# Performance work log

Measured on AMD Instinct MI355X. Metric: run time of the kernel, lower is better.

## Reference

```python
import jax, jax.numpy as jnp
import numpy as np

EMBED_DIM = 1024
NUM_HEADS = 16
HEAD_DIM = EMBED_DIM // NUM_HEADS
B, T = 4, 2048


def setup_inputs() -> dict:
    key = jax.random.key(0)
    ks = jax.random.split(key, 5)
    s = 1.0 / np.sqrt(EMBED_DIM)
    x = jax.random.normal(ks[0], (B, T, EMBED_DIM), dtype=jnp.float32)
    W_qkv = jax.random.uniform(ks[1], (EMBED_DIM, 3 * EMBED_DIM), minval=-s, maxval=s, dtype=jnp.float32)
    b_qkv = jax.random.uniform(ks[2], (3 * EMBED_DIM,), minval=-s, maxval=s, dtype=jnp.float32)
    W_proj = jax.random.uniform(ks[3], (EMBED_DIM, EMBED_DIM), minval=-s, maxval=s, dtype=jnp.float32)
    b_proj = jax.random.uniform(ks[4], (EMBED_DIM,), minval=-s, maxval=s, dtype=jnp.float32)
    return {"x": x, "W_qkv": W_qkv, "b_qkv": b_qkv, "W_proj": W_proj, "b_proj": b_proj}


def reference(x, W_qkv, b_qkv, W_proj, b_proj):
    Bq, Tq, C = x.shape
    H, D = NUM_HEADS, HEAD_DIM
    qkv = x @ W_qkv + b_qkv                      # [B,T,3C]
    qkv = qkv.reshape(Bq, Tq, 3, H, D)
    q = qkv[:, :, 0].transpose(0, 2, 1, 3)       # [B,H,T,D]
    k = qkv[:, :, 1].transpose(0, 2, 1, 3)
    v = qkv[:, :, 2].transpose(0, 2, 1, 3)
    scale = 1.0 / jnp.sqrt(jnp.asarray(D, x.dtype))
    attn = jnp.einsum('bhqd,bhkd->bhqk', q, k) * scale  # [B,H,T,T]
    mask = jnp.tril(jnp.ones((Tq, Tq), dtype=bool))     # causal: keep lower triangle
    attn = jnp.where(mask, attn, jnp.asarray(-jnp.inf, attn.dtype))
    attn = jax.nn.softmax(attn, axis=-1)
    out = jnp.einsum('bhqk,bhkd->bhqd', attn, v)        # [B,H,T,D]
    out = out.transpose(0, 2, 1, 3).reshape(Bq, Tq, C)
    return out @ W_proj + b_proj
```

## Files before the change

### kernel.cpp

```cpp
#include <hip/hip_runtime.h>
#include <stdint.h>

typedef unsigned short ushort_t;
typedef __attribute__((ext_vector_type(4))) unsigned int  u32x4;
typedef __attribute__((ext_vector_type(2))) unsigned int  u32x2;
typedef __attribute__((ext_vector_type(4))) float         f32x4;
typedef __attribute__((ext_vector_type(8))) __bf16        bf16x8;
typedef __attribute__((ext_vector_type(2))) __bf16        bf16x2;

__device__ __forceinline__ ushort_t f2bf(float f) {
    unsigned int u = __float_as_uint(f);
    u += 0x7fffu + ((u >> 16) & 1u);
    return (ushort_t)(u >> 16);
}
__device__ __forceinline__ unsigned int pack2bf(float a, float b) {
    return (unsigned int)f2bf(a) | ((unsigned int)f2bf(b) << 16);
}
#if __has_builtin(__builtin_amdgcn_cvt_pk_bf16_f32)
__device__ __forceinline__ unsigned int pack2bf_fast(float a, float b) {
    bf16x2 v = __builtin_amdgcn_cvt_pk_bf16_f32(a, b);
    return __builtin_bit_cast(unsigned int, v);
}
#else
__device__ __forceinline__ unsigned int pack2bf_fast(float a, float b) {
    return pack2bf(a, b);
}
#endif
__device__ __forceinline__ f32x4 mfma16(bf16x8 a, bf16x8 b, f32x4 c) {
    return __builtin_amdgcn_mfma_f32_16x16x32_bf16(a, b, c, 0, 0, 0);
}
__device__ __forceinline__ bf16x8 ldfrag(const ushort_t* p) {
    return __builtin_bit_cast(bf16x8, *(const u32x4*)p);
}

__device__ __forceinline__ void wg_barrier() {
    asm volatile("s_waitcnt lgkmcnt(0)\n\ts_barrier" ::: "memory");
}

#define QSCALE 0.18033688011112042f

__global__ __launch_bounds__(256) void xcast(const float* __restrict__ X,
                                             ushort_t* __restrict__ Xb) {
    long i = ((long)blockIdx.x * 256 + threadIdx.x) * 8;
    float4 a = *(const float4*)(X + i);
    float4 b = *(const float4*)(X + i + 4);
    u32x4 pk;
    pk.x = pack2bf(a.x, a.y); pk.y = pack2bf(a.z, a.w);
    pk.z = pack2bf(b.x, b.y); pk.w = pack2bf(b.z, b.w);
    *(u32x4*)(Xb + i) = pk;
}

__global__ __launch_bounds__(256) void wt_kernel(const float* __restrict__ W,
                                                 ushort_t* __restrict__ Wt,
                                                 int K, int N) {
    __shared__ float tile[32][33];
    int tx = threadIdx.x, ty = threadIdx.y;
    int n0 = blockIdx.x * 32, k0 = blockIdx.y * 32;
    for (int p = 0; p < 4; ++p)
        tile[ty + 8*p][tx] = W[(long)(k0 + ty + 8*p) * N + n0 + tx];
    __syncthreads();
    for (int p = 0; p < 4; ++p)
        Wt[(long)(n0 + ty + 8*p) * K + k0 + tx] = f2bf(tile[tx][ty + 8*p]);
}

__global__ __launch_bounds__(256) void gemm_qkv(const ushort_t* __restrict__ Xb,
                                                const ushort_t* __restrict__ Wt,
                                                const float* __restrict__ bias,
                                                ushort_t* __restrict__ Qo,
                                                ushort_t* __restrict__ Ko,
                                                ushort_t* __restrict__ Vto) {
    __shared__ __align__(16) ushort_t smem[128 * 136];

    const int tid  = threadIdx.x;
    const int g    = blockIdx.x;
    const int grp  = g / 192, rr = g % 192;
    const int m0   = (grp * 8 + (rr & 7)) * 128;
    const int n0   = (rr >> 3) * 128;
    const int lane = tid & 63, w = tid >> 6;
    const int quad = lane >> 4, l16 = lane & 15;
    const int wm = (w >> 1) * 64, wn = (w & 1) * 64;

    const int srow  = tid >> 2;
    const int slot  = tid & 3;
    const int oct   = slot ^ ((tid >> 3) & 3);
    const int wofs  = srow * 32 + slot * 8;
    const int rslot = (quad ^ ((l16 >> 1) & 3)) * 8;

    const ushort_t* Ap = Xb + (long)(m0 + srow) * 1024 + oct * 8;
    const ushort_t* Bp = Wt + (long)(n0 + srow) * 1024 + oct * 8;

    f32x4 acc[4][4] = {};

    u32x4 AA0 = *(const u32x4*)(Ap);
    u32x4 AA1 = *(const u32x4*)(Ap + 65536);
    u32x4 BA0 = *(const u32x4*)(Bp);
    u32x4 BA1 = *(const u32x4*)(Bp + 65536);
    u32x4 AB0 = *(const u32x4*)(Ap + 32);
    u32x4 AB1 = *(const u32x4*)(Ap + 32 + 65536);
    u32x4 BB0 = *(const u32x4*)(Bp + 32);
    u32x4 BB1 = *(const u32x4*)(Bp + 32 + 65536);

    for (int k0 = 0; k0 < 1024; k0 += 64) {
        {
            ushort_t* As = smem;
            ushort_t* Bs = smem + 8192;
            *(u32x4*)&As[wofs]        = AA0;
            *(u32x4*)&As[wofs + 2048] = AA1;
            *(u32x4*)&Bs[wofs]        = BA0;
            *(u32x4*)&Bs[wofs + 2048] = BA1;
            int kf = (k0 + 64 < 1024) ? k0 + 64 : k0;
            AA0 = *(const u32x4*)(Ap + kf);
            AA1 = *(const u32x4*)(Ap + kf + 65536);
            BA0 = *(const u32x4*)(Bp + kf);
            BA1 = *(const u32x4*)(Bp + kf + 65536);
            wg_barrier();
            bf16x8 af[4], bfr[4];
            for (int i = 0; i < 4; ++i)
                af[i] = ldfrag(&As[(wm + 16*i + l16) * 32 + rslot]);
            for (int j = 0; j < 4; ++j)
                bfr[j] = ldfrag(&Bs[(wn + 16*j + l16) * 32 + rslot]);
            for (int i = 0; i < 4; ++i)
                for (int j = 0; j < 4; ++j)
                    acc[i][j] = mfma16(af[i], bfr[j], acc[i][j]);
        }
        {
            ushort_t* As = smem + 4096;
            ushort_t* Bs = smem + 8192 + 4096;
            *(u32x4*)&As[wofs]        = AB0;
            *(u32x4*)&As[wofs + 2048] = AB1;
            *(u32x4*)&Bs[wofs]        = BB0;
            *(u32x4*)&Bs[wofs + 2048] = BB1;
            int kf = (k0 + 96 < 1024) ? k0 + 96 : k0 + 32;
            AB0 = *(const u32x4*)(Ap + kf);
            AB1 = *(const u32x4*)(Ap + kf + 65536);
            BB0 = *(const u32x4*)(Bp + kf);
            BB1 = *(const u32x4*)(Bp + kf + 65536);
            wg_barrier();
            bf16x8 af[4], bfr[4];
            for (int i = 0; i < 4; ++i)
                af[i] = ldfrag(&As[(wm + 16*i + l16) * 32 + rslot]);
            for (int j = 0; j < 4; ++j)
                bfr[j] = ldfrag(&Bs[(wn + 16*j + l16) * 32 + rslot]);
            for (int i = 0; i < 4; ++i)
                for (int j = 0; j < 4; ++j)
                    acc[i][j] = mfma16(af[i], bfr[j], acc[i][j]);
        }
    }

    float bj[4];
    for (int j = 0; j < 4; ++j) bj[j] = bias[n0 + wn + 16*j + l16];
    const int bb = m0 >> 11, t0m = m0 & 2047;
    __syncthreads();

    if (n0 < 2048) {
        ushort_t* dst = (n0 < 1024) ? Qo : Ko;
        const float scale = (n0 < 1024) ? QSCALE : 1.0f;
        const int nbase = (n0 < 1024) ? n0 : n0 - 1024;
        for (int i = 0; i < 4; ++i)
            for (int j = 0; j < 4; ++j) {
                int nl = wn + 16*j + l16;
                for (int r = 0; r < 4; ++r) {
                    int ml = wm + 16*i + quad*4 + r;
                    smem[ml * 136 + nl] = f2bf((acc[i][j][r] + bj[j]) * scale);
                }
            }
        __syncthreads();
        for (int c = 0; c < 8; ++c) {
            int chunk = tid + 256 * c;
            int row = chunk >> 4, nc = (chunk & 15) * 8;
            int n = nbase + nc;
            int hh = n >> 6, d = n & 63;
            *(u32x4*)&dst[((long)(bb*16 + hh) * 2048 + t0m + row) * 64 + d] =
                *(const u32x4*)&smem[row * 136 + nc];
        }
    } else {
        for (int i = 0; i < 4; ++i)
            for (int j = 0; j < 4; ++j) {
                int nl = wn + 16*j + l16;
                for (int r = 0; r < 4; ++r) {
                    int ml = wm + 16*i + quad*4 + r;
                    smem[nl * 136 + ml] = f2bf(acc[i][j][r] + bj[j]);
                }
            }
        __syncthreads();
        for (int c = 0; c < 8; ++c) {
            int chunk = tid + 256 * c;
            int row = chunk >> 4, mc = (chunk & 15) * 8;
            int n = n0 - 2048 + row;
            int hh = n >> 6, d = n & 63;
            *(u32x4*)&Vto[((long)(bb*16 + hh) * 64 + d) * 2048 + t0m + mc] =
                *(const u32x4*)&smem[row * 136 + mc];
        }
    }
}

__global__ __launch_bounds__(256) void attn_kernel(const ushort_t* __restrict__ Q,
                                                   const ushort_t* __restrict__ K,
                                                   const ushort_t* __restrict__ Vt,
                                                   ushort_t* __restrict__ O) {
    __shared__ __align__(16) ushort_t Ks[2][64 * 64];
    __shared__ __align__(16) ushort_t Vs[2][64 * 64];
    __shared__ __align__(16) ushort_t Ps[128 * 72];

    const int tid  = threadIdx.x;
    const int lane = tid & 63, w = tid >> 6, quad = lane >> 4, l16 = lane & 15;
    const int g    = blockIdx.x;
    const int bh   = (g & 7) + 8 * ((g >> 3) & 7);
    const int qt   = 15 - (g >> 6);
    const ushort_t* qptr = Q  + (long)bh * 2048 * 64;
    const ushort_t* kptr = K  + (long)bh * 2048 * 64;
    const ushort_t* vptr = Vt + (long)bh * 64 * 2048;
    const int bb2 = bh >> 4, h = bh & 15;

    const int srow = tid >> 3;
    const int slot = tid & 7;
    const int oct  = slot ^ (srow & 7);
    const int koff = srow * 64 + oct * 8;
    const int voff = srow * 2048 + oct * 8;
    const int wofs = srow * 64 + slot * 8;

    const int qbase = qt * 128;
    const int nkt = 2 * qt + 2;

    for (int c = 0; c < 4; ++c) {
        int flat = tid + 256 * c;
        int row = flat >> 3, kc = (flat & 7) * 8;
        *(u32x4*)&Ps[row * 72 + kc] = *(const u32x4*)&qptr[(long)(qbase + row) * 64 + kc];
    }
    wg_barrier();
    bf16x8 qf[2][2];
    for (int nt = 0; nt < 2; ++nt)
        for (int kk = 0; kk < 2; ++kk)
            qf[nt][kk] = ldfrag(&Ps[(32*w + 16*nt + l16) * 72 + kk*32 + quad*8]);

    f32x4 acc[2][4] = {};
    float l_run[2] = {0.f, 0.f};

    auto phase = [&](int kt, ushort_t* Kb, ushort_t* Vb) {
        const int kbase = kt * 64;
        if (kbase > qbase + 32*w + 31) return;
        f32x4 s[4][2] = {};
        __builtin_amdgcn_s_setprio(1);
        for (int kk = 0; kk < 2; ++kk)
            for (int mt = 0; mt < 4; ++mt) {
                bf16x8 kf = ldfrag(&Kb[(16*mt + l16) * 64 + ((4*kk + quad) ^ (l16 & 7)) * 8]);
                for (int nt = 0; nt < 2; ++nt)
                    s[mt][nt] = mfma16(kf, qf[nt][kk], s[mt][nt]);
            }
        __builtin_amdgcn_s_setprio(0);
        if (kbase + 63 > qbase + 32*w) {
            for (int mt = 0; mt < 4; ++mt)
                for (int nt = 0; nt < 2; ++nt) {
                    int qv = qbase + 32*w + 16*nt + l16;
                    for (int r = 0; r < 4; ++r)
                        if (kbase + 16*mt + 4*quad + r > qv)
                            s[mt][nt][r] = -__builtin_inff();
                }
        }
        for (int nt = 0; nt < 2; ++nt)
            for (int mt = 0; mt < 4; ++mt) {
                float p0 = __builtin_amdgcn_exp2f(s[mt][nt][0]);
                float p1 = __builtin_amdgcn_exp2f(s[mt][nt][1]);
                float p2 = __builtin_amdgcn_exp2f(s[mt][nt][2]);
                float p3 = __builtin_amdgcn_exp2f(s[mt][nt][3]);
                l_run[nt] += (p0 + p1) + (p2 + p3);
                u32x2 pk;
                pk.x = pack2bf_fast(p0, p1);
                pk.y = pack2bf_fast(p2, p3);
                *(u32x2*)&Ps[(32*w + 16*nt + l16) * 72 + 16*mt + 4*quad] = pk;
            }
        __builtin_amdgcn_s_setprio(1);
        for (int kk = 0; kk < 2; ++kk) {
            bf16x8 pf0 = ldfrag(&Ps[(32*w + l16) * 72 + kk*32 + quad*8]);
            bf16x8 pf1 = ldfrag(&Ps[(32*w + 16 + l16) * 72 + kk*32 + quad*8]);
            for (int jd = 0; jd < 4; ++jd) {
                bf16x8 vf = ldfrag(&Vb[(16*jd + l16) * 64 + ((4*kk + quad) ^ (l16 & 7)) * 8]);
                acc[0][jd] = mfma16(pf0, vf, acc[0][jd]);
                acc[1][jd] = mfma16(pf1, vf, acc[1][jd]);
            }
        }
        __builtin_amdgcn_s_setprio(0);
    };

    u32x4 KA0 = *(const u32x4*)(kptr + koff);
    u32x4 KA1 = *(const u32x4*)(kptr + koff + 2048);
    u32x4 VA0 = *(const u32x4*)(vptr + voff);
    u32x4 VA1 = *(const u32x4*)(vptr + voff + 65536);
    u32x4 KB0 = *(const u32x4*)(kptr + 4096 + koff);
    u32x4 KB1 = *(const u32x4*)(kptr + 4096 + koff + 2048);
    u32x4 VB0 = *(const u32x4*)(vptr + 64 + voff);
    u32x4 VB1 = *(const u32x4*)(vptr + 64 + voff + 65536);

    for (int kt = 0; kt < nkt; kt += 2) {
        {
            *(u32x4*)&Ks[0][wofs]        = KA0;
            *(u32x4*)&Ks[0][wofs + 2048] = KA1;
            *(u32x4*)&Vs[0][wofs]        = VA0;
            *(u32x4*)&Vs[0][wofs + 2048] = VA1;
            int kf = (kt + 2 < nkt) ? kt + 2 : kt;
            KA0 = *(const u32x4*)(kptr + kf*4096 + koff);
            KA1 = *(const u32x4*)(kptr + kf*4096 + koff + 2048);
            VA0 = *(const u32x4*)(vptr + kf*64 + voff);
            VA1 = *(const u32x4*)(vptr + kf*64 + voff + 65536);
            wg_barrier();
            phase(kt, Ks[0], Vs[0]);
        }
        {
            *(u32x4*)&Ks[1][wofs]        = KB0;
            *(u32x4*)&Ks[1][wofs + 2048] = KB1;
            *(u32x4*)&Vs[1][wofs]        = VB0;
            *(u32x4*)&Vs[1][wofs + 2048] = VB1;
            int kf = (kt + 3 < nkt) ? kt + 3 : kt + 1;
            KB0 = *(const u32x4*)(kptr + kf*4096 + koff);
            KB1 = *(const u32x4*)(kptr + kf*4096 + koff + 2048);
            VB0 = *(const u32x4*)(vptr + kf*64 + voff);
            VB1 = *(const u32x4*)(vptr + kf*64 + voff + 65536);
            wg_barrier();
            phase(kt + 1, Ks[1], Vs[1]);
        }
    }

    for (int i = 0; i < 2; ++i) {
        float l = l_run[i];
        l += __shfl_xor(l, 16, 64);
        l += __shfl_xor(l, 32, 64);
        for (int r = 0; r < 4; ++r) {
            float linv = 1.0f / __shfl(l, (lane & 48) | (4*quad + r), 64);
            int t = qbase + 32*w + 16*i + 4*quad + r;
            for (int jd = 0; jd < 4; ++jd) {
                int d = 16*jd + l16;
                O[((long)(bb2*2048 + t)) * 1024 + h*64 + d] = f2bf(acc[i][jd][r] * linv);
            }
        }
    }
}

__global__ __launch_bounds__(256) void gemm_proj(const ushort_t* __restrict__ A,
                                                 const ushort_t* __restrict__ Wt,
                                                 const float* __restrict__ bias,
                                                 float* __restrict__ Out) {
    __shared__ __align__(16) ushort_t smem[4 * 4096];

    const int tid  = threadIdx.x;
    const int g    = blockIdx.x;
    const int grp  = g / 64, rr = g % 64;
    const int m0   = (grp * 8 + (rr & 7)) * 128;
    const int n0   = (rr >> 3) * 128;
    const int lane = tid & 63, w = tid >> 6;
    const int quad = lane >> 4, l16 = lane & 15;
    const int wm = (w >> 1) * 64, wn = (w & 1) * 64;

    const int srow  = tid >> 2;
    const int slot  = tid & 3;
    const int oct   = slot ^ ((tid >> 3) & 3);
    const int wofs  = srow * 32 + slot * 8;
    const int rslot = (quad ^ ((l16 >> 1) & 3)) * 8;

    const ushort_t* Ap = A  + (long)(m0 + srow) * 1024 + oct * 8;
    const ushort_t* Bp = Wt + (long)(n0 + srow) * 1024 + oct * 8;

    f32x4 acc[4][4] = {};

    u32x4 AA0 = *(const u32x4*)(Ap);
    u32x4 AA1 = *(const u32x4*)(Ap + 65536);
    u32x4 BA0 = *(const u32x4*)(Bp);
    u32x4 BA1 = *(const u32x4*)(Bp + 65536);
    u32x4 AB0 = *(const u32x4*)(Ap + 32);
    u32x4 AB1 = *(const u32x4*)(Ap + 32 + 65536);
    u32x4 BB0 = *(const u32x4*)(Bp + 32);
    u32x4 BB1 = *(const u32x4*)(Bp + 32 + 65536);

    for (int k0 = 0; k0 < 1024; k0 += 64) {
        {
            ushort_t* As = smem;
            ushort_t* Bs = smem + 8192;
            *(u32x4*)&As[wofs]        = AA0;
            *(u32x4*)&As[wofs + 2048] = AA1;
            *(u32x4*)&Bs[wofs]        = BA0;
            *(u32x4*)&Bs[wofs + 2048] = BA1;
            int kf = (k0 + 64 < 1024) ? k0 + 64 : k0;
            AA0 = *(const u32x4*)(Ap + kf);
            AA1 = *(const u32x4*)(Ap + kf + 65536);
            BA0 = *(const u32x4*)(Bp + kf);
            BA1 = *(const u32x4*)(Bp + kf + 65536);
            wg_barrier();
            bf16x8 af[4], bfr[4];
            for (int i = 0; i < 4; ++i)
                af[i] = ldfrag(&As[(wm + 16*i + l16) * 32 + rslot]);
            for (int j = 0; j < 4; ++j)
                bfr[j] = ldfrag(&Bs[(wn + 16*j + l16) * 32 + rslot]);
            for (int i = 0; i < 4; ++i)
                for (int j = 0; j < 4; ++j)
                    acc[i][j] = mfma16(af[i], bfr[j], acc[i][j]);
        }
        {
            ushort_t* As = smem + 4096;
            ushort_t* Bs = smem + 8192 + 4096;
            *(u32x4*)&As[wofs]        = AB0;
            *(u32x4*)&As[wofs + 2048] = AB1;
            *(u32x4*)&Bs[wofs]        = BB0;
            *(u32x4*)&Bs[wofs + 2048] = BB1;
            int kf = (k0 + 96 < 1024) ? k0 + 96 : k0 + 32;
            AB0 = *(const u32x4*)(Ap + kf);
            AB1 = *(const u32x4*)(Ap + kf + 65536);
            BB0 = *(const u32x4*)(Bp + kf);
            BB1 = *(const u32x4*)(Bp + kf + 65536);
            wg_barrier();
            bf16x8 af[4], bfr[4];
            for (int i = 0; i < 4; ++i)
                af[i] = ldfrag(&As[(wm + 16*i + l16) * 32 + rslot]);
            for (int j = 0; j < 4; ++j)
                bfr[j] = ldfrag(&Bs[(wn + 16*j + l16) * 32 + rslot]);
            for (int i = 0; i < 4; ++i)
                for (int j = 0; j < 4; ++j)
                    acc[i][j] = mfma16(af[i], bfr[j], acc[i][j]);
        }
    }

    float bj[4];
    for (int j = 0; j < 4; ++j) bj[j] = bias[n0 + wn + 16*j + l16];
    for (int i = 0; i < 4; ++i)
        for (int j = 0; j < 4; ++j)
            for (int r = 0; r < 4; ++r) {
                int m = m0 + wm + 16*i + quad*4 + r;
                int n = n0 + wn + 16*j + l16;
                Out[(long)m * 1024 + n] = acc[i][j][r] + bj[j];
            }
}

extern "C" void kernel_launch(void* const* d_in, const int* in_sizes, int n_in,
                              void* d_out, int out_size, void* d_ws, size_t ws_size,
                              hipStream_t stream) {
    const float* x     = (const float*)d_in[0];
    const float* Wqkv  = (const float*)d_in[1];
    const float* bqkv  = (const float*)d_in[2];
    const float* Wproj = (const float*)d_in[3];
    const float* bproj = (const float*)d_in[4];
    float* out = (float*)d_out;

    ushort_t* wqkvt  = (ushort_t*)d_ws;
    ushort_t* wprojt = wqkvt  + 3072 * 1024;
    ushort_t* Qb     = wprojt + 1024 * 1024;
    ushort_t* Kb     = Qb  + 8388608;
    ushort_t* Vtb    = Kb  + 8388608;
    ushort_t* XbA2   = Vtb + 8388608;

    xcast<<<4096, 256, 0, stream>>>(x, XbA2);
    wt_kernel<<<dim3(96, 32), dim3(32, 8), 0, stream>>>(Wqkv, wqkvt, 1024, 3072);
    wt_kernel<<<dim3(32, 32), dim3(32, 8), 0, stream>>>(Wproj, wprojt, 1024, 1024);
    gemm_qkv<<<1536, 256, 0, stream>>>(XbA2, wqkvt, bqkv, Qb, Kb, Vtb);
    attn_kernel<<<1024, 256, 0, stream>>>(Qb, Kb, Vtb, XbA2);
    gemm_proj<<<512, 256, 0, stream>>>(XbA2, wprojt, bproj, out);
}
```

Measured before the change: 244.9 us.

## Use direct global-to-LDS loads with triple-buffered pipeline in GEMMs, merge prep kernels

Both GEMM kernels now use global_load_lds to copy A/B tiles straight into shared memory, with a three-stage ring buffer and vmcnt-based waits replacing register-staged double buffering. MFMA sections get raised wave priority. The three prep kernels (x cast and two weight transposes) are merged into one launch. This aims to cut register pressure, VGPR-to-LDS store instructions and launch overhead, at the cost of more LDS per block and reliance on correct wait counts for the async loads.

```diff
diff --git a/kernel.cpp b/kernel.cpp
--- a/kernel.cpp
+++ b/kernel.cpp
@@ -33,34 +33,47 @@
     return __builtin_bit_cast(bf16x8, *(const u32x4*)p);
 }
 
+__device__ __forceinline__ void gld16(const ushort_t* g, ushort_t* l) {
+    __builtin_amdgcn_global_load_lds(
+        (const __attribute__((address_space(1))) void*)g,
+        (__attribute__((address_space(3))) void*)l, 16, 0, 0);
+}
+
 __device__ __forceinline__ void wg_barrier() {
     asm volatile("s_waitcnt lgkmcnt(0)\n\ts_barrier" ::: "memory");
 }
 
 #define QSCALE 0.18033688011112042f
 
-__global__ __launch_bounds__(256) void xcast(const float* __restrict__ X,
-                                             ushort_t* __restrict__ Xb) {
-    long i = ((long)blockIdx.x * 256 + threadIdx.x) * 8;
-    float4 a = *(const float4*)(X + i);
-    float4 b = *(const float4*)(X + i + 4);
-    u32x4 pk;
-    pk.x = pack2bf(a.x, a.y); pk.y = pack2bf(a.z, a.w);
-    pk.z = pack2bf(b.x, b.y); pk.w = pack2bf(b.z, b.w);
-    *(u32x4*)(Xb + i) = pk;
-}
-
-__global__ __launch_bounds__(256) void wt_kernel(const float* __restrict__ W,
-                                                 ushort_t* __restrict__ Wt,
-                                                 int K, int N) {
+__global__ __launch_bounds__(256) void prep(const float* __restrict__ X,
+                                            ushort_t* __restrict__ Xb,
+                                            const float* __restrict__ Wq,
+                                            ushort_t* __restrict__ Wqt,
+                                            const float* __restrict__ Wp,
+                                            ushort_t* __restrict__ Wpt) {
     __shared__ float tile[32][33];
-    int tx = threadIdx.x, ty = threadIdx.y;
-    int n0 = blockIdx.x * 32, k0 = blockIdx.y * 32;
+    const int tid = threadIdx.x;
+    const int b   = blockIdx.x;
+    if (b < 4096) {
+        long i = ((long)b * 256 + tid) * 8;
+        float4 a = *(const float4*)(X + i);
+        float4 c = *(const float4*)(X + i + 4);
+        u32x4 pk;
+        pk.x = pack2bf(a.x, a.y); pk.y = pack2bf(a.z, a.w);
+        pk.z = pack2bf(c.x, c.y); pk.w = pack2bf(c.z, c.w);
+        *(u32x4*)(Xb + i) = pk;
+        return;
+    }
+    const float* W; ushort_t* Wt; int N, bx, by;
+    if (b < 7168) { int idx = b - 4096; W = Wq; Wt = Wqt; N = 3072; bx = idx % 96; by = idx / 96; }
+    else          { int idx = b - 7168; W = Wp; Wt = Wpt; N = 1024; bx = idx & 31; by = idx >> 5; }
+    const int tx = tid & 31, ty = tid >> 5;
+    const int n0 = bx * 32, k0 = by * 32;
     for (int p = 0; p < 4; ++p)
         tile[ty + 8*p][tx] = W[(long)(k0 + ty + 8*p) * N + n0 + tx];
     __syncthreads();
     for (int p = 0; p < 4; ++p)
-        Wt[(long)(n0 + ty + 8*p) * K + k0 + tx] = f2bf(tile[tx][ty + 8*p]);
+        Wt[(long)(n0 + ty + 8*p) * 1024 + k0 + tx] = f2bf(tile[tx][ty + 8*p]);
 }
 
 __global__ __launch_bounds__(256) void gemm_qkv(const ushort_t* __restrict__ Xb,
@@ -69,7 +82,7 @@
                                                 ushort_t* __restrict__ Qo,
                                                 ushort_t* __restrict__ Ko,
                                                 ushort_t* __restrict__ Vto) {
-    __shared__ __align__(16) ushort_t smem[128 * 136];
+    __shared__ __align__(16) ushort_t smem[24576];
 
     const int tid  = threadIdx.x;
     const int g    = blockIdx.x;
@@ -83,73 +96,52 @@
     const int srow  = tid >> 2;
     const int slot  = tid & 3;
     const int oct   = slot ^ ((tid >> 3) & 3);
-    const int wofs  = srow * 32 + slot * 8;
     const int rslot = (quad ^ ((l16 >> 1) & 3)) * 8;
+    const int wbase = (tid & 192) * 8;
 
     const ushort_t* Ap = Xb + (long)(m0 + srow) * 1024 + oct * 8;
     const ushort_t* Bp = Wt + (long)(n0 + srow) * 1024 + oct * 8;
 
     f32x4 acc[4][4] = {};
 
-    u32x4 AA0 = *(const u32x4*)(Ap);
-    u32x4 AA1 = *(const u32x4*)(Ap + 65536);
-    u32x4 BA0 = *(const u32x4*)(Bp);
-    u32x4 BA1 = *(const u32x4*)(Bp + 65536);
-    u32x4 AB0 = *(const u32x4*)(Ap + 32);
-    u32x4 AB1 = *(const u32x4*)(Ap + 32 + 65536);
-    u32x4 BB0 = *(const u32x4*)(Bp + 32);
-    u32x4 BB1 = *(const u32x4*)(Bp + 32 + 65536);
-
-    for (int k0 = 0; k0 < 1024; k0 += 64) {
-        {
-            ushort_t* As = smem;
-            ushort_t* Bs = smem + 8192;
-            *(u32x4*)&As[wofs]        = AA0;
-            *(u32x4*)&As[wofs + 2048] = AA1;
-            *(u32x4*)&Bs[wofs]        = BA0;
-            *(u32x4*)&Bs[wofs + 2048] = BA1;
-            int kf = (k0 + 64 < 1024) ? k0 + 64 : k0;
-            AA0 = *(const u32x4*)(Ap + kf);
-            AA1 = *(const u32x4*)(Ap + kf + 65536);
-            BA0 = *(const u32x4*)(Bp + kf);
-            BA1 = *(const u32x4*)(Bp + kf + 65536);
-            wg_barrier();
-            bf16x8 af[4], bfr[4];
-            for (int i = 0; i < 4; ++i)
-                af[i] = ldfrag(&As[(wm + 16*i + l16) * 32 + rslot]);
+    auto issue = [&](int pf, int ibuf) {
+        int k = (pf < 32) ? (pf << 5) : 0;
+        gld16(Ap + k,         &smem[ibuf + wbase]);
+        gld16(Ap + k + 65536, &smem[ibuf + wbase + 2048]);
+        gld16(Bp + k,         &smem[ibuf + wbase + 4096]);
+        gld16(Bp + k + 65536, &smem[ibuf + wbase + 6144]);
+    };
+    auto step = [&](int p, int rbuf, int ibuf) {
+        asm volatile("s_waitcnt vmcnt(4)\n\ts_barrier" ::: "memory");
+        issue(p + 2, ibuf);
+        const ushort_t* As = smem + rbuf;
+        const ushort_t* Bs = As + 4096;
+        bf16x8 af[4], bfr[4];
+        for (int i = 0; i < 4; ++i)
+            af[i] = ldfrag(&As[(wm + 16*i + l16) * 32 + rslot]);
+        for (int j = 0; j < 4; ++j)
+            bfr[j] = ldfrag(&Bs[(wn + 16*j + l16) * 32 + rslot]);
+        __builtin_amdgcn_s_setprio(1);
+        for (int i = 0; i < 4; ++i)
             for (int j = 0; j < 4; ++j)
-                bfr[j] = ldfrag(&Bs[(wn + 16*j + l16) * 32 + rslot]);
-            for (int i = 0; i < 4; ++i)
-                for (int j = 0; j < 4; ++j)
-                    acc[i][j] = mfma16(af[i], bfr[j], acc[i][j]);
-        }
-        {
-            ushort_t* As = smem + 4096;
-            ushort_t* Bs = smem + 8192 + 4096;
-            *(u32x4*)&As[wofs]        = AB0;
-            *(u32x4*)&As[wofs + 2048] = AB1;
-            *(u32x4*)&Bs[wofs]        = BB0;
-            *(u32x4*)&Bs[wofs + 2048] = BB1;
-            int kf = (k0 + 96 < 1024) ? k0 + 96 : k0 + 32;
-            AB0 = *(const u32x4*)(Ap + kf);
-            AB1 = *(const u32x4*)(Ap + kf + 65536);
-            BB0 = *(const u32x4*)(Bp + kf);
-            BB1 = *(const u32x4*)(Bp + kf + 65536);
-            wg_barrier();
-            bf16x8 af[4], bfr[4];
-            for (int i = 0; i < 4; ++i)
-                af[i] = ldfrag(&As[(wm + 16*i + l16) * 32 + rslot]);
-            for (int j = 0; j < 4; ++j)
-                bfr[j] = ldfrag(&Bs[(wn + 16*j + l16) * 32 + rslot]);
-            for (int i = 0; i < 4; ++i)
-                for (int j = 0; j < 4; ++j)
-                    acc[i][j] = mfma16(af[i], bfr[j], acc[i][j]);
-        }
-    }
+                acc[i][j] = mfma16(af[i], bfr[j], acc[i][j]);
+        __builtin_amdgcn_s_setprio(0);
+    };
+
+    issue(0, 0);
+    issue(1, 8192);
+    for (int p = 0; p < 30; p += 3) {
+        step(p,     0,     16384);
+        step(p + 1, 8192,  0);
+        step(p + 2, 16384, 8192);
+    }
+    step(30, 0,    16384);
+    step(31, 8192, 0);
 
     float bj[4];
     for (int j = 0; j < 4; ++j) bj[j] = bias[n0 + wn + 16*j + l16];
     const int bb = m0 >> 11, t0m = m0 & 2047;
+    asm volatile("s_waitcnt vmcnt(0)" ::: "memory");
     __syncthreads();
 
     if (n0 < 2048) {
@@ -339,7 +331,7 @@
                                                  const ushort_t* __restrict__ Wt,
                                                  const float* __restrict__ bias,
                                                  float* __restrict__ Out) {
-    __shared__ __align__(16) ushort_t smem[4 * 4096];
+    __shared__ __align__(16) ushort_t smem[24576];
 
     const int tid  = threadIdx.x;
     const int g    = blockIdx.x;
@@ -353,69 +345,48 @@
     const int srow  = tid >> 2;
     const int slot  = tid & 3;
     const int oct   = slot ^ ((tid >> 3) & 3);
-    const int wofs  = srow * 32 + slot * 8;
     const int rslot = (quad ^ ((l16 >> 1) & 3)) * 8;
+    const int wbase = (tid & 192) * 8;
 
     const ushort_t* Ap = A  + (long)(m0 + srow) * 1024 + oct * 8;
     const ushort_t* Bp = Wt + (long)(n0 + srow) * 1024 + oct * 8;
 
     f32x4 acc[4][4] = {};
 
-    u32x4 AA0 = *(const u32x4*)(Ap);
-    u32x4 AA1 = *(const u32x4*)(Ap + 65536);
-    u32x4 BA0 = *(const u32x4*)(Bp);
-    u32x4 BA1 = *(const u32x4*)(Bp + 65536);
-    u32x4 AB0 = *(const u32x4*)(Ap + 32);
-    u32x4 AB1 = *(const u32x4*)(Ap + 32 + 65536);
-    u32x4 BB0 = *(const u32x4*)(Bp + 32);
-    u32x4 BB1 = *(const u32x4*)(Bp + 32 + 65536);
-
-    for (int k0 = 0; k0 < 1024; k0 += 64) {
-        {
-            ushort_t* As = smem;
-            ushort_t* Bs = smem + 8192;
-            *(u32x4*)&As[wofs]        = AA0;
-            *(u32x4*)&As[wofs + 2048] = AA1;
-            *(u32x4*)&Bs[wofs]        = BA0;
-            *(u32x4*)&Bs[wofs + 2048] = BA1;
-            int kf = (k0 + 64 < 1024) ? k0 + 64 : k0;
-            AA0 = *(const u32x4*)(Ap + kf);
-            AA1 = *(const u32x4*)(Ap + kf + 65536);
-            BA0 = *(const u32x4*)(Bp + kf);
-            BA1 = *(const u32x4*)(Bp + kf + 65536);
-            wg_barrier();
-            bf16x8 af[4], bfr[4];
-            for (int i = 0; i < 4; ++i)
-                af[i] = ldfrag(&As[(wm + 16*i + l16) * 32 + rslot]);
+    auto issue = [&](int pf, int ibuf) {
+        int k = (pf < 32) ? (pf << 5) : 0;
+        gld16(Ap + k,         &smem[ibuf + wbase]);
+        gld16(Ap + k + 65536, &smem[ibuf + wbase + 2048]);
+        gld16(Bp + k,         &smem[ibuf + wbase + 4096]);
+        gld16(Bp + k + 65536, &smem[ibuf + wbase + 6144]);
+    };
+    auto step = [&](int p, int rbuf, int ibuf) {
+        asm volatile("s_waitcnt vmcnt(4)\n\ts_barrier" ::: "memory");
+        issue(p + 2, ibuf);
+        const ushort_t* As = smem + rbuf;
+        const ushort_t* Bs = As + 4096;
+        bf16x8 af[4], bfr[4];
+        for (int i = 0; i < 4; ++i)
+            af[i] = ldfrag(&As[(wm + 16*i + l16) * 32 + rslot]);
+        for (int j = 0; j < 4; ++j)
+            bfr[j] = ldfrag(&Bs[(wn + 16*j + l16) * 32 + rslot]);
+        __builtin_amdgcn_s_setprio(1);
+        for (int i = 0; i < 4; ++i)
             for (int j = 0; j < 4; ++j)
-                bfr[j] = ldfrag(&Bs[(wn + 16*j + l16) * 32 + rslot]);
-            for (int i = 0; i < 4; ++i)
-                for (int j = 0; j < 4; ++j)
-                    acc[i][j] = mfma16(af[i], bfr[j], acc[i][j]);
-        }
-        {
-            ushort_t* As = smem + 4096;
-            ushort_t* Bs = smem + 8192 + 4096;
-            *(u32x4*)&As[wofs]        = AB0;
-            *(u32x4*)&As[wofs + 2048] = AB1;
-            *(u32x4*)&Bs[wofs]        = BB0;
-            *(u32x4*)&Bs[wofs + 2048] = BB1;
-            int kf = (k0 + 96 < 1024) ? k0 + 96 : k0 + 32;
-            AB0 = *(const u32x4*)(Ap + kf);
-            AB1 = *(const u32x4*)(Ap + kf + 65536);
-            BB0 = *(const u32x4*)(Bp + kf);
-            BB1 = *(const u32x4*)(Bp + kf + 65536);
-            wg_barrier();
-            bf16x8 af[4], bfr[4];
-            for (int i = 0; i < 4; ++i)
-                af[i] = ldfrag(&As[(wm + 16*i + l16) * 32 + rslot]);
-            for (int j = 0; j < 4; ++j)
-                bfr[j] = ldfrag(&Bs[(wn + 16*j + l16) * 32 + rslot]);
-            for (int i = 0; i < 4; ++i)
-                for (int j = 0; j < 4; ++j)
-                    acc[i][j] = mfma16(af[i], bfr[j], acc[i][j]);
-        }
-    }
+                acc[i][j] = mfma16(af[i], bfr[j], acc[i][j]);
+        __builtin_amdgcn_s_setprio(0);
+    };
+
+    issue(0, 0);
+    issue(1, 8192);
+    for (int p = 0; p < 30; p += 3) {
+        step(p,     0,     16384);
+        step(p + 1, 8192,  0);
+        step(p + 2, 16384, 8192);
+    }
+    step(30, 0,    16384);
+    step(31, 8192, 0);
+    asm volatile("s_waitcnt vmcnt(0)" ::: "memory");
 
     float bj[4];
     for (int j = 0; j < 4; ++j) bj[j] = bias[n0 + wn + 16*j + l16];
@@ -445,9 +416,7 @@
     ushort_t* Vtb    = Kb  + 8388608;
     ushort_t* XbA2   = Vtb + 8388608;
 
-    xcast<<<4096, 256, 0, stream>>>(x, XbA2);
-    wt_kernel<<<dim3(96, 32), dim3(32, 8), 0, stream>>>(Wqkv, wqkvt, 1024, 3072);
-    wt_kernel<<<dim3(32, 32), dim3(32, 8), 0, stream>>>(Wproj, wprojt, 1024, 1024);
+    prep<<<8192, 256, 0, stream>>>(x, XbA2, Wqkv, wqkvt, Wproj, wprojt);
     gemm_qkv<<<1536, 256, 0, stream>>>(XbA2, wqkvt, bqkv, Qb, Kb, Vtb);
     attn_kernel<<<1024, 256, 0, stream>>>(Qb, Kb, Vtb, XbA2);
     gemm_proj<<<512, 256, 0, stream>>>(XbA2, wprojt, bproj, out);
```

Result: no change. 242.4 us (-1.0%).
